# Kernel tuning notes

Hardware: AMD Instinct MI355X
Metric: run time of the kernel (lower is better)

The kernel has to match this reference:

```python
import jax, jax.numpy as jnp
import numpy as np

B, S, HID = 1, 2048, 2048
H, KVH, D = 16, 8, 128
N_REP = H // KVH
SCALING = float(np.sqrt(D))  # head_dim ** 0.5 (nGPT uses positive exponent)
SQK_INIT_VALUE = 1.0
SQK_INIT_SCALING = 0.02
EPS = 1e-8


def _rotate_half(x):
    x1, x2 = jnp.split(x, 2, axis=-1)
    return jnp.concatenate((-x2, x1), axis=-1)


def setup_inputs() -> dict:
    key = jax.random.key(0)
    ks = jax.random.split(key, 8)
    hidden_states = jax.random.normal(ks[0], (B, S, HID), dtype=jnp.float32)
    # realistic RoPE tables, full rotary (rotary_dim == head_dim)
    inv_freq = 1.0 / (10000.0 ** (np.arange(0, D, 2, dtype=np.float32) / D))
    t = np.arange(S, dtype=np.float32)
    freqs = np.outer(t, inv_freq)                      # [S, D/2]
    emb = np.concatenate([freqs, freqs], axis=-1)      # [S, D]
    cos = jnp.asarray(np.cos(emb))[None].repeat(B, 0)  # [B, S, D]
    sin = jnp.asarray(np.sin(emb))[None].repeat(B, 0)
    # additive causal mask [B, 1, S, S]
    causal = jnp.tril(jnp.ones((S, S), dtype=bool))
    attention_mask = jnp.where(causal, 0.0, jnp.finfo(jnp.float32).min)[None, None].repeat(B, 0)
    sd = 0.02
    Wq = jax.random.normal(ks[1], (H * D, HID), dtype=jnp.float32) * sd
    Wk = jax.random.normal(ks[2], (KVH * D, HID), dtype=jnp.float32) * sd
    Wv = jax.random.normal(ks[3], (KVH * D, HID), dtype=jnp.float32) * sd
    Wo = jax.random.normal(ks[4], (HID, H * D), dtype=jnp.float32) * sd
    sqk_w = jnp.full((H * D,), SQK_INIT_SCALING, dtype=jnp.float32)  # Linear(1, H*D) weight, init constant
    return {"hidden_states": hidden_states, "cos": cos, "sin": sin,
            "attention_mask": attention_mask, "Wq": Wq, "Wk": Wk, "Wv": Wv,
            "Wo": Wo, "sqk_w": sqk_w}


def _l2_normalize(x):
    return x / (jnp.linalg.norm(x, axis=-1, keepdims=True) + EPS)


def reference(hidden_states, cos, sin, attention_mask, Wq, Wk, Wv, Wo, sqk_w):
    b, s, _ = hidden_states.shape
    # projections (torch Linear: y = x @ W.T)
    q = jnp.einsum('bsd,ed->bse', hidden_states, Wq).reshape(b, s, H, D).transpose(0, 2, 1, 3)
    k = jnp.einsum('bsd,ed->bse', hidden_states, Wk).reshape(b, s, KVH, D).transpose(0, 2, 1, 3)
    v = jnp.einsum('bsd,ed->bse', hidden_states, Wv).reshape(b, s, KVH, D).transpose(0, 2, 1, 3)
    # RoPE, cos/sin broadcast over heads: [B,1,S,D]
    c, sn = cos[:, None], sin[:, None]
    q = q * c + _rotate_half(q) * sn
    k = k * c + _rotate_half(k) * sn
    # nGPT: L2-normalize q,k; learnable per-channel scale on q
    sqk = (sqk_w * (SQK_INIT_VALUE / SQK_INIT_SCALING)).reshape(1, H, 1, D)
    q = _l2_normalize(q) * sqk ** 2
    k = _l2_normalize(k)
    # GQA: repeat kv heads
    k = jnp.repeat(k, N_REP, axis=1)
    v = jnp.repeat(v, N_REP, axis=1)
    scores = jnp.einsum('bhqd,bhkd->bhqk', q, k) * SCALING
    scores = scores + attention_mask
    attn = jax.nn.softmax(scores.astype(jnp.float32), axis=-1).astype(q.dtype)
    out = jnp.einsum('bhqk,bhkd->bhqd', attn, v)
    out = out.transpose(0, 2, 1, 3).reshape(b, s, H * D)
    return jnp.einsum('bse,de->bsd', out, Wo)
```

## Files before the change

### kernel.cpp

```cpp
#include <hip/hip_runtime.h>

typedef unsigned short u16;
typedef __attribute__((ext_vector_type(4))) float f32x4;
typedef __attribute__((ext_vector_type(16))) float f32x16;
typedef __attribute__((ext_vector_type(8))) __bf16 bf16x8;
typedef __attribute__((ext_vector_type(8))) u16 u16x8;
typedef __attribute__((ext_vector_type(4))) u16 u16x4;
typedef __attribute__((ext_vector_type(4))) unsigned int u32x4;

#define S_LEN 2048
#define NH 16
#define NKV 8
#define QSCALE_LOG2E 16.322118857f
#define M2INIT 16.6f
#define EXP2(x) __builtin_amdgcn_exp2f(x)

#define SWZK(r) (((((r) & 7) << 4)) ^ (((((r) >> 3) & 1)) << 7))
#define SWZV(r) (((((r) & 7) << 4)) ^ (((((r) >> 3) & 1)) << 6))

#define AS1(p) ((const __attribute__((address_space(1))) void*)(p))
#define AS3(p) ((__attribute__((address_space(3))) void*)(p))

#define PIPE_WAIT6() asm volatile("s_waitcnt vmcnt(6)\ns_barrier" ::: "memory")
#define PIPE_WAIT4() asm volatile("s_waitcnt vmcnt(4)\ns_barrier" ::: "memory")
#define PIPE_WAIT0() asm volatile("s_waitcnt vmcnt(0)\ns_barrier" ::: "memory")

__device__ __forceinline__ float b2f(u16 u) {
    return __uint_as_float(((unsigned int)u) << 16);
}
__device__ __forceinline__ u16 f2b(float f) {
    unsigned int x = __float_as_uint(f);
    unsigned int r = (x + 0x7FFFu + ((x >> 16) & 1u)) >> 16;
    return (u16)r;
}

__global__ __launch_bounds__(256) void cast_all(const float* __restrict__ hs,
                                                const float* __restrict__ Wq,
                                                const float* __restrict__ Wk,
                                                const float* __restrict__ Wv,
                                                const float* __restrict__ Wo,
                                                u16* __restrict__ hsb,
                                                u16* __restrict__ wcat,
                                                u16* __restrict__ wob) {
    int i = blockIdx.x * 256 + threadIdx.x;
    const float* src; u16* dst; int off;
    if (i < 1048576)      { src = hs; dst = hsb;            off = i; }
    else if (i < 2097152) { src = Wq; dst = wcat;           off = i - 1048576; }
    else if (i < 2621440) { src = Wk; dst = wcat + 4194304; off = i - 2097152; }
    else if (i < 3145728) { src = Wv; dst = wcat + 6291456; off = i - 2621440; }
    else                  { src = Wo; dst = wob;            off = i - 3145728; }
    f32x4 v = reinterpret_cast<const f32x4*>(src)[off];
    u16x4 o;
    o[0] = f2b(v[0]); o[1] = f2b(v[1]); o[2] = f2b(v[2]); o[3] = f2b(v[3]);
    reinterpret_cast<u16x4*>(dst)[off] = o;
}

__global__ __launch_bounds__(512) void gemm_qkv(const u16* __restrict__ A,
                                                const u16* __restrict__ B,
                                                const float* __restrict__ cosb,
                                                const float* __restrict__ sinb,
                                                const float* __restrict__ sqkw,
                                                u16* __restrict__ qb,
                                                u16* __restrict__ kb,
                                                u16* __restrict__ vt) {
    const int K = 2048;
    __shared__ alignas(16) u16 As[3][128 * 64];
    __shared__ alignas(16) u16 Bs[3][256 * 64];
    int tid = threadIdx.x, lane = tid & 63, wave = tid >> 6;
    int row0 = blockIdx.y * 128, col0 = blockIdx.x * 256;
    int wr = (wave >> 1) * 32;
    int wc = (wave & 1) * 128;
    int l15 = lane & 15, lg = lane >> 4;

    f32x4 acc[2][8] = {};

    auto stage = [&](int bf, int k0) {
#pragma unroll
        for (int i = 0; i < 2; i++) {
            int slot = i * 8 + wave;
            int r = slot * 8 + (lane >> 3);
            int c = (lane & 7) ^ (r & 7);
            __builtin_amdgcn_global_load_lds(AS1(A + (size_t)(row0 + r) * K + k0 + c * 8),
                                             AS3(&As[bf][slot * 512]), 16, 0, 0);
        }
#pragma unroll
        for (int i = 0; i < 4; i++) {
            int slot = i * 8 + wave;
            int r = slot * 8 + (lane >> 3);
            int c = (lane & 7) ^ (r & 7);
            __builtin_amdgcn_global_load_lds(AS1(B + (size_t)(col0 + r) * K + k0 + c * 8),
                                             AS3(&Bs[bf][slot * 512]), 16, 0, 0);
        }
    };

    const int nk = K >> 6;
    stage(0, 0);
    stage(1, 64);

    for (int t = 0; t < nk; ++t) {
        int buf = t % 3;
        __builtin_amdgcn_sched_barrier(0);
        if (t + 1 < nk) PIPE_WAIT6(); else PIPE_WAIT0();
        if (t + 2 < nk) stage((t + 2) % 3, (t + 2) * 64);

        __builtin_amdgcn_s_setprio(1);
#pragma unroll
        for (int kk = 0; kk < 2; kk++) {
            bf16x8 af[2], bg[8];
#pragma unroll
            for (int m = 0; m < 2; m++) {
                int r = wr + m * 16 + l15;
                af[m] = *reinterpret_cast<const bf16x8*>(&As[buf][r * 64 + (((kk * 4 + lg) ^ (r & 7)) * 8)]);
            }
#pragma unroll
            for (int n = 0; n < 8; n++) {
                int r = wc + n * 16 + l15;
                bg[n] = *reinterpret_cast<const bf16x8*>(&Bs[buf][r * 64 + (((kk * 4 + lg) ^ (r & 7)) * 8)]);
            }
#pragma unroll
            for (int m = 0; m < 2; m++)
#pragma unroll
                for (int n = 0; n < 8; n++)
                    acc[m][n] = __builtin_amdgcn_mfma_f32_16x16x32_bf16(af[m], bg[n], acc[m][n], 0, 0, 0);
        }
        __builtin_amdgcn_s_setprio(0);
    }

    int c32 = blockIdx.x * 2 + (wave & 1);
    if (c32 < 24) {
        bool isQ = c32 < 16;
        float w2[8];
        if (isQ) {
#pragma unroll
            for (int j = 0; j < 8; j++) {
                float w = sqkw[c32 * 128 + j * 16 + l15] * 50.f;
                w2[j] = w * w * QSCALE_LOG2E;
            }
        }
        u16* outb = isQ ? (qb + (size_t)c32 * S_LEN * 128)
                        : (kb + (size_t)(c32 - 16) * S_LEN * 128);
#pragma unroll
        for (int m = 0; m < 2; m++)
#pragma unroll
            for (int r = 0; r < 4; r++) {
                int s = row0 + wr + m * 16 + lg * 4 + r;
                const float* crow = cosb + (size_t)s * 128;
                const float* srow = sinb + (size_t)s * 128;
                float y[8];
                float ss = 0.f;
#pragma unroll
                for (int j = 0; j < 4; j++) {
                    float c  = crow[j * 16 + l15];
                    float sn = srow[j * 16 + l15];
                    float x0 = acc[m][j][r], x1 = acc[m][j + 4][r];
                    float a = x0 * c - x1 * sn;
                    float b = x1 * c + x0 * sn;
                    y[j] = a; y[j + 4] = b;
                    ss += a * a + b * b;
                }
                ss += __shfl_xor(ss, 1);
                ss += __shfl_xor(ss, 2);
                ss += __shfl_xor(ss, 4);
                ss += __shfl_xor(ss, 8);
                float inv = 1.f / (sqrtf(ss) + 1e-8f);
                u16* orow = outb + (size_t)s * 128;
                if (isQ) {
#pragma unroll
                    for (int j = 0; j < 8; j++)
                        orow[j * 16 + l15] = f2b(y[j] * inv * w2[j]);
                } else {
#pragma unroll
                    for (int j = 0; j < 8; j++)
                        orow[j * 16 + l15] = f2b(y[j] * inv);
                }
            }
    } else {
        int g = c32 - 24;
#pragma unroll
        for (int n = 0; n < 8; n++) {
            int d = n * 16 + l15;
            u16* vrow = vt + (size_t)(g * 128 + d) * S_LEN;
#pragma unroll
            for (int m = 0; m < 2; m++) {
                u16x4 pk;
#pragma unroll
                for (int r = 0; r < 4; r++) pk[r] = f2b(acc[m][n][r]);
                *reinterpret_cast<u16x4*>(&vrow[row0 + wr + m * 16 + lg * 4]) = pk;
            }
        }
    }
}

__global__ __launch_bounds__(512) void gemm_o(const u16* __restrict__ A,
                                              const u16* __restrict__ B,
                                              float* __restrict__ C,
                                              int M, int N, int K) {
    __shared__ alignas(16) u16 As[3][128 * 64];
    __shared__ alignas(16) u16 Bs[3][128 * 64];
    int tid = threadIdx.x, lane = tid & 63, wave = tid >> 6;
    int row0 = blockIdx.y * 128, col0 = blockIdx.x * 128;
    int wr = (wave >> 1) * 32;
    int wc = (wave & 1) * 64;
    int l15 = lane & 15, lg = lane >> 4;

    f32x4 acc[2][4] = {};

    auto stage = [&](int bf, int k0) {
#pragma unroll
        for (int i = 0; i < 2; i++) {
            int slot = i * 8 + wave;
            int r = slot * 8 + (lane >> 3);
            int c = (lane & 7) ^ (r & 7);
            __builtin_amdgcn_global_load_lds(AS1(A + (size_t)(row0 + r) * K + k0 + c * 8),
                                             AS3(&As[bf][slot * 512]), 16, 0, 0);
        }
#pragma unroll
        for (int i = 0; i < 2; i++) {
            int slot = i * 8 + wave;
            int r = slot * 8 + (lane >> 3);
            int c = (lane & 7) ^ (r & 7);
            __builtin_amdgcn_global_load_lds(AS1(B + (size_t)(col0 + r) * K + k0 + c * 8),
                                             AS3(&Bs[bf][slot * 512]), 16, 0, 0);
        }
    };

    const int nk = K >> 6;
    stage(0, 0);
    stage(1, 64);

    for (int t = 0; t < nk; ++t) {
        int buf = t % 3;
        __builtin_amdgcn_sched_barrier(0);
        if (t + 1 < nk) PIPE_WAIT4(); else PIPE_WAIT0();
        if (t + 2 < nk) stage((t + 2) % 3, (t + 2) * 64);

        __builtin_amdgcn_s_setprio(1);
#pragma unroll
        for (int kk = 0; kk < 2; kk++) {
            bf16x8 af[2], bg[4];
#pragma unroll
            for (int m = 0; m < 2; m++) {
                int r = wr + m * 16 + l15;
                af[m] = *reinterpret_cast<const bf16x8*>(&As[buf][r * 64 + (((kk * 4 + lg) ^ (r & 7)) * 8)]);
            }
#pragma unroll
            for (int n = 0; n < 4; n++) {
                int r = wc + n * 16 + l15;
                bg[n] = *reinterpret_cast<const bf16x8*>(&Bs[buf][r * 64 + (((kk * 4 + lg) ^ (r & 7)) * 8)]);
            }
#pragma unroll
            for (int m = 0; m < 2; m++)
#pragma unroll
                for (int n = 0; n < 4; n++)
                    acc[m][n] = __builtin_amdgcn_mfma_f32_16x16x32_bf16(af[m], bg[n], acc[m][n], 0, 0, 0);
        }
        __builtin_amdgcn_s_setprio(0);
    }

#pragma unroll
    for (int m = 0; m < 2; m++)
#pragma unroll
        for (int n = 0; n < 4; n++)
#pragma unroll
            for (int r = 0; r < 4; r++) {
                int row = row0 + wr + m * 16 + lg * 4 + r;
                int col = col0 + wc + n * 16 + l15;
                C[(size_t)row * N + col] = acc[m][n][r];
            }
}

__global__ __launch_bounds__(256) void attn_mfma(const u16* __restrict__ Qb,
                                                 const u16* __restrict__ Kb,
                                                 const u16* __restrict__ Vt,
                                                 u16* __restrict__ Ao) {
    __shared__ alignas(16) char smem[50432];
    u16* Ks = (u16*)smem;
    u16* Vs = (u16*)(smem + 16384);
    float* scrO = (float*)smem;
    float* scrL = (float*)(smem + 32768);
    u16*   scrT = (u16*)(smem + 33024);

    int tid = threadIdx.x, lane = tid & 63, wv = tid >> 6;
    int h = blockIdx.x & (NH - 1);
    int z = blockIdx.x >> 4;
    int qi = (z < 16) ? (31 - z) : (z - 16);
    int qb0 = qi * 64;
    int g = h >> 1;
    int l31 = lane & 31, hi = lane >> 5;
    int qoff = (wv >> 1) * 32, koff = (wv & 1) * 32;
    int qabs = qb0 + qoff + l31;

    bf16x8 qf[8];
    {
        const u16* qrow = Qb + ((size_t)h * S_LEN + qabs) * 128;
#pragma unroll
        for (int kd = 0; kd < 8; kd++)
            qf[kd] = *reinterpret_cast<const bf16x8*>(qrow + kd * 16 + hi * 8);
    }

    const u16* kbase = Kb + (size_t)g * S_LEN * 128;
    const u16* vbase = Vt + (size_t)g * 128 * S_LEN;

    int rk = wv * 16 + (lane >> 4);
    int ck = lane & 15;
    int rv = wv * 32 + (lane >> 3);
    int cv = lane & 7;

    u16x8 kreg[4], vreg[4];
    f32x16 oacc[4] = {};
    float lpart = 0.f;

    int nt = qi + 1;

#pragma unroll
    for (int i = 0; i < 4; i++) {
        kreg[i] = *reinterpret_cast<const u16x8*>(kbase + (size_t)(rk + 4 * i) * 128 + ck * 8);
        vreg[i] = *reinterpret_cast<const u16x8*>(vbase + (size_t)(rv + 8 * i) * S_LEN + cv * 8);
    }

    for (int t = 0; t < nt; ++t) {
        int k0 = t * 64;
        __syncthreads();
#pragma unroll
        for (int i = 0; i < 4; i++) {
            int r = rk + 4 * i;
            *reinterpret_cast<u16x8*>((char*)Ks + r * 256 + ((ck * 16) ^ SWZK(r))) = kreg[i];
            int r2 = rv + 8 * i;
            *reinterpret_cast<u16x8*>((char*)Vs + r2 * 128 + ((cv * 16) ^ SWZV(r2))) = vreg[i];
        }
        __syncthreads();

        if (t + 1 < nt) {
            int kn = k0 + 64;
#pragma unroll
            for (int i = 0; i < 4; i++) {
                kreg[i] = *reinterpret_cast<const u16x8*>(kbase + (size_t)(kn + rk + 4 * i) * 128 + ck * 8);
                vreg[i] = *reinterpret_cast<const u16x8*>(vbase + (size_t)(rv + 8 * i) * S_LEN + kn + cv * 8);
            }
        }

        f32x16 s0 = {}, s1 = {};
        int krow = koff + l31;
        char* krp = (char*)Ks + krow * 256;
        int ksw = SWZK(krow);
        __builtin_amdgcn_s_setprio(1);
#pragma unroll
        for (int kd = 0; kd < 8; kd += 2) {
            bf16x8 kf0 = *reinterpret_cast<const bf16x8*>(krp + ((kd * 32 + hi * 16) ^ ksw));
            bf16x8 kf1 = *reinterpret_cast<const bf16x8*>(krp + (((kd + 1) * 32 + hi * 16) ^ ksw));
            s0 = __builtin_amdgcn_mfma_f32_32x32x16_bf16(kf0, qf[kd], s0, 0, 0, 0);
            s1 = __builtin_amdgcn_mfma_f32_32x32x16_bf16(kf1, qf[kd + 1], s1, 0, 0, 0);
        }
        __builtin_amdgcn_s_setprio(0);

        float p[16];
        bool maskt = (t == nt - 1);
#pragma unroll
        for (int r = 0; r < 16; r++) {
            float s = s0[r] + s1[r];
            if (maskt) {
                int key = k0 + koff + (r & 3) + 8 * (r >> 2) + 4 * hi;
                if (key > qabs) s = -1e30f;
            }
            float pv = EXP2(s - M2INIT);
            p[r] = pv;
            lpart += pv;
        }

        bf16x8 pf[2];
#pragma unroll
        for (int ks = 0; ks < 2; ks++) {
            int b = ks * 8;
            unsigned int A0 = (unsigned int)f2b(p[b + 0]) | ((unsigned int)f2b(p[b + 1]) << 16);
            unsigned int A1 = (unsigned int)f2b(p[b + 2]) | ((unsigned int)f2b(p[b + 3]) << 16);
            unsigned int A2 = (unsigned int)f2b(p[b + 4]) | ((unsigned int)f2b(p[b + 5]) << 16);
            unsigned int A3 = (unsigned int)f2b(p[b + 6]) | ((unsigned int)f2b(p[b + 7]) << 16);
            unsigned int S0 = __shfl_xor(A0, 32);
            unsigned int S1 = __shfl_xor(A1, 32);
            unsigned int S2 = __shfl_xor(A2, 32);
            unsigned int S3 = __shfl_xor(A3, 32);
            u32x4 w;
            w[0] = hi ? S2 : A0;
            w[1] = hi ? S3 : A1;
            w[2] = hi ? A2 : S0;
            w[3] = hi ? A3 : S1;
            pf[ks] = *reinterpret_cast<bf16x8*>(&w);
        }

        __builtin_amdgcn_s_setprio(1);
#pragma unroll
        for (int db = 0; db < 4; db++) {
            int vr = db * 32 + l31;
            char* vrp = (char*)Vs + vr * 128;
            int vsw = SWZV(vr);
#pragma unroll
            for (int ks = 0; ks < 2; ks++) {
                bf16x8 vf = *reinterpret_cast<const bf16x8*>(vrp + ((koff * 2 + ks * 32 + hi * 16) ^ vsw));
                oacc[db] = __builtin_amdgcn_mfma_f32_32x32x16_bf16(vf, pf[ks], oacc[db], 0, 0, 0);
            }
        }
        __builtin_amdgcn_s_setprio(0);
    }

    float lw = lpart + __shfl_xor(lpart, 32);
    int rg = wv >> 1;
    __syncthreads();
    if (wv & 1) {
#pragma unroll
        for (int db = 0; db < 4; db++)
#pragma unroll
            for (int r = 0; r < 16; r++) {
                int d = db * 32 + (r & 3) + 8 * (r >> 2) + 4 * hi;
                scrO[(rg * 128 + d) * 32 + l31] = oacc[db][r];
            }
        if (lane < 32) scrL[rg * 32 + l31] = lw;
    }
    __syncthreads();
    if (!(wv & 1)) {
        float inv = 1.f / (lw + scrL[rg * 32 + l31]);
#pragma unroll
        for (int db = 0; db < 4; db++)
#pragma unroll
            for (int r = 0; r < 16; r++) {
                int d = db * 32 + (r & 3) + 8 * (r >> 2) + 4 * hi;
                float o = (oacc[db][r] + scrO[(rg * 128 + d) * 32 + l31]) * inv;
                scrT[(rg * 32 + l31) * 136 + d] = f2b(o);
            }
    }
    __syncthreads();
    for (int i = tid; i < 64 * 16; i += 256) {
        int q = i >> 4, c = i & 15;
        u16x8 v = *reinterpret_cast<const u16x8*>(&scrT[q * 136 + c * 8]);
        *reinterpret_cast<u16x8*>(&Ao[(size_t)(qb0 + q) * 2048 + h * 128 + c * 8]) = v;
    }
}

extern "C" void kernel_launch(void* const* d_in, const int* in_sizes, int n_in,
                              void* d_out, int out_size, void* d_ws, size_t ws_size,
                              hipStream_t stream) {
    const float* hs   = (const float*)d_in[0];
    const float* cosb = (const float*)d_in[1];
    const float* sinb = (const float*)d_in[2];
    const float* Wq   = (const float*)d_in[4];
    const float* Wk   = (const float*)d_in[5];
    const float* Wv   = (const float*)d_in[6];
    const float* Wo   = (const float*)d_in[7];
    const float* sqkw = (const float*)d_in[8];

    char* ws = (char*)d_ws;
    u16*   hsb  = (u16*)(ws);
    u16*   wcat = (u16*)(ws + 8388608);
    u16*   wob  = (u16*)(ws + 25165824);
    u16*   qb   = (u16*)(ws + 33554432);
    u16*   kb   = (u16*)(ws + 41943040);
    u16*   vt   = (u16*)(ws + 46137344);
    u16*   ao   = (u16*)(ws + 50331648);

    cast_all<<<16384, 256, 0, stream>>>(hs, Wq, Wk, Wv, Wo, hsb, wcat, wob);

    gemm_qkv<<<dim3(16, 16), 512, 0, stream>>>(hsb, wcat, cosb, sinb, sqkw, qb, kb, vt);

    attn_mfma<<<512, 256, 0, stream>>>(qb, kb, vt, ao);

    gemm_o<<<dim3(16, 16), 512, 0, stream>>>(ao, wob, (float*)d_out, 2048, 2048, 2048);
}
```

Measured before the change: 148.7 us.

## Load K/V fragments directly from global in attention and retile output GEMM

The attention kernel stops staging K and V tiles through shared memory with two barriers per tile. Each wave now loads its K fragments straight into registers, prefetched one tile ahead, and its V fragments straight from global memory per tile. This removes the LDS round-trip and block-level syncs but adds redundant global/L2 traffic, because the wave pairs sharing koff and the two heads in a GQA group each reload the same data. Separately, the output GEMM moves to 128x64 tiles with 256 threads and twice as many blocks, with the pipeline wait count adjusted to match.

```diff
diff --git a/kernel.cpp b/kernel.cpp
--- a/kernel.cpp
+++ b/kernel.cpp
@@ -15,14 +15,10 @@
 #define M2INIT 16.6f
 #define EXP2(x) __builtin_amdgcn_exp2f(x)
 
-#define SWZK(r) (((((r) & 7) << 4)) ^ (((((r) >> 3) & 1)) << 7))
-#define SWZV(r) (((((r) & 7) << 4)) ^ (((((r) >> 3) & 1)) << 6))
-
 #define AS1(p) ((const __attribute__((address_space(1))) void*)(p))
 #define AS3(p) ((__attribute__((address_space(3))) void*)(p))
 
 #define PIPE_WAIT6() asm volatile("s_waitcnt vmcnt(6)\ns_barrier" ::: "memory")
-#define PIPE_WAIT4() asm volatile("s_waitcnt vmcnt(4)\ns_barrier" ::: "memory")
 #define PIPE_WAIT0() asm volatile("s_waitcnt vmcnt(0)\ns_barrier" ::: "memory")
 
 __device__ __forceinline__ float b2f(u16 u) {
@@ -191,24 +187,23 @@
     }
 }
 
-__global__ __launch_bounds__(512) void gemm_o(const u16* __restrict__ A,
+__global__ __launch_bounds__(256) void gemm_o(const u16* __restrict__ A,
                                               const u16* __restrict__ B,
                                               float* __restrict__ C,
                                               int M, int N, int K) {
     __shared__ alignas(16) u16 As[3][128 * 64];
-    __shared__ alignas(16) u16 Bs[3][128 * 64];
+    __shared__ alignas(16) u16 Bs[3][64 * 64];
     int tid = threadIdx.x, lane = tid & 63, wave = tid >> 6;
-    int row0 = blockIdx.y * 128, col0 = blockIdx.x * 128;
-    int wr = (wave >> 1) * 32;
-    int wc = (wave & 1) * 64;
+    int row0 = blockIdx.y * 128, col0 = blockIdx.x * 64;
+    int wr = wave * 32;
     int l15 = lane & 15, lg = lane >> 4;
 
     f32x4 acc[2][4] = {};
 
     auto stage = [&](int bf, int k0) {
 #pragma unroll
-        for (int i = 0; i < 2; i++) {
-            int slot = i * 8 + wave;
+        for (int i = 0; i < 4; i++) {
+            int slot = i * 4 + wave;
             int r = slot * 8 + (lane >> 3);
             int c = (lane & 7) ^ (r & 7);
             __builtin_amdgcn_global_load_lds(AS1(A + (size_t)(row0 + r) * K + k0 + c * 8),
@@ -216,7 +211,7 @@
         }
 #pragma unroll
         for (int i = 0; i < 2; i++) {
-            int slot = i * 8 + wave;
+            int slot = i * 4 + wave;
             int r = slot * 8 + (lane >> 3);
             int c = (lane & 7) ^ (r & 7);
             __builtin_amdgcn_global_load_lds(AS1(B + (size_t)(col0 + r) * K + k0 + c * 8),
@@ -231,7 +226,7 @@
     for (int t = 0; t < nk; ++t) {
         int buf = t % 3;
         __builtin_amdgcn_sched_barrier(0);
-        if (t + 1 < nk) PIPE_WAIT4(); else PIPE_WAIT0();
+        if (t + 1 < nk) PIPE_WAIT6(); else PIPE_WAIT0();
         if (t + 2 < nk) stage((t + 2) % 3, (t + 2) * 64);
 
         __builtin_amdgcn_s_setprio(1);
@@ -245,7 +240,7 @@
             }
 #pragma unroll
             for (int n = 0; n < 4; n++) {
-                int r = wc + n * 16 + l15;
+                int r = n * 16 + l15;
                 bg[n] = *reinterpret_cast<const bf16x8*>(&Bs[buf][r * 64 + (((kk * 4 + lg) ^ (r & 7)) * 8)]);
             }
 #pragma unroll
@@ -264,7 +259,7 @@
 #pragma unroll
             for (int r = 0; r < 4; r++) {
                 int row = row0 + wr + m * 16 + lg * 4 + r;
-                int col = col0 + wc + n * 16 + l15;
+                int col = col0 + n * 16 + l15;
                 C[(size_t)row * N + col] = acc[m][n][r];
             }
 }
@@ -274,8 +269,6 @@
                                                  const u16* __restrict__ Vt,
                                                  u16* __restrict__ Ao) {
     __shared__ alignas(16) char smem[50432];
-    u16* Ks = (u16*)smem;
-    u16* Vs = (u16*)(smem + 16384);
     float* scrO = (float*)smem;
     float* scrL = (float*)(smem + 32768);
     u16*   scrT = (u16*)(smem + 33024);
@@ -301,57 +294,44 @@
     const u16* kbase = Kb + (size_t)g * S_LEN * 128;
     const u16* vbase = Vt + (size_t)g * 128 * S_LEN;
 
-    int rk = wv * 16 + (lane >> 4);
-    int ck = lane & 15;
-    int rv = wv * 32 + (lane >> 3);
-    int cv = lane & 7;
-
-    u16x8 kreg[4], vreg[4];
     f32x16 oacc[4] = {};
     float lpart = 0.f;
-
     int nt = qi + 1;
 
-#pragma unroll
-    for (int i = 0; i < 4; i++) {
-        kreg[i] = *reinterpret_cast<const u16x8*>(kbase + (size_t)(rk + 4 * i) * 128 + ck * 8);
-        vreg[i] = *reinterpret_cast<const u16x8*>(vbase + (size_t)(rv + 8 * i) * S_LEN + cv * 8);
+    u16x8 kreg[8];
+    {
+        const u16* kr = kbase + (size_t)(koff + l31) * 128 + hi * 8;
+#pragma unroll
+        for (int kd = 0; kd < 8; kd++)
+            kreg[kd] = *reinterpret_cast<const u16x8*>(kr + kd * 16);
     }
 
     for (int t = 0; t < nt; ++t) {
-        int k0 = t * 64;
-        __syncthreads();
-#pragma unroll
-        for (int i = 0; i < 4; i++) {
-            int r = rk + 4 * i;
-            *reinterpret_cast<u16x8*>((char*)Ks + r * 256 + ((ck * 16) ^ SWZK(r))) = kreg[i];
-            int r2 = rv + 8 * i;
-            *reinterpret_cast<u16x8*>((char*)Vs + r2 * 128 + ((cv * 16) ^ SWZV(r2))) = vreg[i];
-        }
-        __syncthreads();
+        int kstart = t * 64 + koff;
+
+        f32x16 s0 = {}, s1 = {};
+        __builtin_amdgcn_s_setprio(1);
+#pragma unroll
+        for (int kd = 0; kd < 8; kd += 2) {
+            s0 = __builtin_amdgcn_mfma_f32_32x32x16_bf16(__builtin_bit_cast(bf16x8, kreg[kd]),     qf[kd],     s0, 0, 0, 0);
+            s1 = __builtin_amdgcn_mfma_f32_32x32x16_bf16(__builtin_bit_cast(bf16x8, kreg[kd + 1]), qf[kd + 1], s1, 0, 0, 0);
+        }
+        __builtin_amdgcn_s_setprio(0);
 
         if (t + 1 < nt) {
-            int kn = k0 + 64;
-#pragma unroll
-            for (int i = 0; i < 4; i++) {
-                kreg[i] = *reinterpret_cast<const u16x8*>(kbase + (size_t)(kn + rk + 4 * i) * 128 + ck * 8);
-                vreg[i] = *reinterpret_cast<const u16x8*>(vbase + (size_t)(rv + 8 * i) * S_LEN + kn + cv * 8);
-            }
-        }
-
-        f32x16 s0 = {}, s1 = {};
-        int krow = koff + l31;
-        char* krp = (char*)Ks + krow * 256;
-        int ksw = SWZK(krow);
-        __builtin_amdgcn_s_setprio(1);
-#pragma unroll
-        for (int kd = 0; kd < 8; kd += 2) {
-            bf16x8 kf0 = *reinterpret_cast<const bf16x8*>(krp + ((kd * 32 + hi * 16) ^ ksw));
-            bf16x8 kf1 = *reinterpret_cast<const bf16x8*>(krp + (((kd + 1) * 32 + hi * 16) ^ ksw));
-            s0 = __builtin_amdgcn_mfma_f32_32x32x16_bf16(kf0, qf[kd], s0, 0, 0, 0);
-            s1 = __builtin_amdgcn_mfma_f32_32x32x16_bf16(kf1, qf[kd + 1], s1, 0, 0, 0);
-        }
-        __builtin_amdgcn_s_setprio(0);
+            const u16* kr = kbase + (size_t)(kstart + 64 + l31) * 128 + hi * 8;
+#pragma unroll
+            for (int kd = 0; kd < 8; kd++)
+                kreg[kd] = *reinterpret_cast<const u16x8*>(kr + kd * 16);
+        }
+
+        u16x8 vreg[8];
+#pragma unroll
+        for (int db = 0; db < 4; db++) {
+            const u16* vr = vbase + (size_t)(db * 32 + l31) * S_LEN + kstart + hi * 8;
+            vreg[db * 2]     = *reinterpret_cast<const u16x8*>(vr);
+            vreg[db * 2 + 1] = *reinterpret_cast<const u16x8*>(vr + 16);
+        }
 
         float p[16];
         bool maskt = (t == nt - 1);
@@ -359,7 +339,7 @@
         for (int r = 0; r < 16; r++) {
             float s = s0[r] + s1[r];
             if (maskt) {
-                int key = k0 + koff + (r & 3) + 8 * (r >> 2) + 4 * hi;
+                int key = kstart + (r & 3) + 8 * (r >> 2) + 4 * hi;
                 if (key > qabs) s = -1e30f;
             }
             float pv = EXP2(s - M2INIT);
@@ -384,20 +364,14 @@
             w[1] = hi ? S3 : A1;
             w[2] = hi ? A2 : S0;
             w[3] = hi ? A3 : S1;
-            pf[ks] = *reinterpret_cast<bf16x8*>(&w);
+            pf[ks] = __builtin_bit_cast(bf16x8, w);
         }
 
         __builtin_amdgcn_s_setprio(1);
 #pragma unroll
         for (int db = 0; db < 4; db++) {
-            int vr = db * 32 + l31;
-            char* vrp = (char*)Vs + vr * 128;
-            int vsw = SWZV(vr);
-#pragma unroll
-            for (int ks = 0; ks < 2; ks++) {
-                bf16x8 vf = *reinterpret_cast<const bf16x8*>(vrp + ((koff * 2 + ks * 32 + hi * 16) ^ vsw));
-                oacc[db] = __builtin_amdgcn_mfma_f32_32x32x16_bf16(vf, pf[ks], oacc[db], 0, 0, 0);
-            }
+            oacc[db] = __builtin_amdgcn_mfma_f32_32x32x16_bf16(__builtin_bit_cast(bf16x8, vreg[db * 2]),     pf[0], oacc[db], 0, 0, 0);
+            oacc[db] = __builtin_amdgcn_mfma_f32_32x32x16_bf16(__builtin_bit_cast(bf16x8, vreg[db * 2 + 1]), pf[1], oacc[db], 0, 0, 0);
         }
         __builtin_amdgcn_s_setprio(0);
     }
@@ -462,5 +436,5 @@
 
     attn_mfma<<<512, 256, 0, stream>>>(qb, kb, vt, ao);
 
-    gemm_o<<<dim3(16, 16), 512, 0, stream>>>(ao, wob, (float*)d_out, 2048, 2048, 2048);
-}
+    gemm_o<<<dim3(32, 16), 256, 0, stream>>>(ao, wob, (float*)d_out, 2048, 2048, 2048);
+}
```

Result: slower. 163.8 us (+10.1%).
